# Kernel optimization log

Hardware: AMD Instinct MI355X
Metric: run time of the kernel (lower is better)

The kernel has to match this reference:

```python
import jax, jax.numpy as jnp
import numpy as np

B, T, D, F, E, K, L, S = 8, 1024, 512, 1024, 8, 2, 2, 64
SE, SH = 64, 128  # subject_embed_dim, style_hidden_dim


def setup_inputs() -> dict:
    key = jax.random.key(0)
    ks = jax.random.split(key, 16)
    r = lambda i, shape, s=0.05: (jax.random.normal(ks[i], shape, jnp.float32) * s)
    return dict(
        x=jax.random.normal(ks[0], (B, T, D), jnp.float32),
        subject_ids=jax.random.randint(ks[1], (B,), 0, S),
        # per-layer LayerNorm params (L, D)
        ln_g=jnp.ones((L, D), jnp.float32), ln_b=jnp.zeros((L, D), jnp.float32),
        # per-layer SubjectStyleAlignment params (weights stored (in, out))
        subj_emb=r(2, (L, S, SE), 0.02),
        h1_w=r(3, (L, SE, SH)), h1_b=jnp.zeros((L, SH), jnp.float32),
        h2_w=r(4, (L, SH, SH)), h2_b=jnp.zeros((L, SH), jnp.float32),
        s1_w=r(5, (L, SH, SH // 2)), s1_b=jnp.zeros((L, SH // 2), jnp.float32),
        s2_w=r(6, (L, SH // 2, 2 * D)), s2_b=jnp.zeros((L, 2 * D), jnp.float32),
        # shared TopKRouter: Linear(D, D//2) -> ReLU -> Linear(D//2, E)
        g1_w=r(7, (D, D // 2)), g1_b=jnp.zeros((D // 2,), jnp.float32),
        g2_w=r(8, (D // 2, E)), g2_b=jnp.zeros((E,), jnp.float32),
        # shared ExpertPool of GLU experts (no bias)
        wi0=r(9, (E, D, F)), wi1=r(10, (E, D, F)), wo=r(11, (E, F, D)),
    )


def _layernorm(x, g, b):
    m = x.mean(-1, keepdims=True)
    v = x.var(-1, keepdims=True)  # biased, matches torch LayerNorm
    return (x - m) / jnp.sqrt(v + 1e-5) * g + b


def reference(x, subject_ids, ln_g, ln_b, subj_emb, h1_w, h1_b, h2_w, h2_b,
              s1_w, s1_b, s2_w, s2_b, g1_w, g1_b, g2_w, g2_b, wi0, wi1, wo):
    Bs, Ts, Ds = x.shape
    for l in range(L):  # small fixed layer loop; expert pool + router are shared
        res = x
        h = _layernorm(x, ln_g[l], ln_b[l])
        # SubjectStyleAlignment: instance norm over time axis per (B, D) channel
        mu = h.mean(1, keepdims=True)
        var = h.var(1, keepdims=True)
        hn = (h - mu) / jnp.sqrt(var + 1e-8)
        e = subj_emb[l][subject_ids]                               # (B, SE)
        hh = jax.nn.relu(e @ h1_w[l] + h1_b[l]) @ h2_w[l] + h2_b[l]
        sp = jax.nn.relu(hh @ s1_w[l] + s1_b[l]) @ s2_w[l] + s2_b[l]  # (B, 2D)
        gamma = jax.nn.softplus(sp[:, :Ds]) + 1e-8
        beta = sp[:, Ds:]
        h = hn * gamma[:, None, :] + beta[:, None, :]
        # Router (shared across layers)
        hf = h.reshape(-1, Ds)                                     # (N, D)
        logits = jax.nn.relu(hf @ g1_w + g1_b) @ g2_w + g2_b       # (N, E)
        probs = jax.nn.softmax(logits, -1)
        gates, idx = jax.lax.top_k(probs, K)                       # (N, K)
        gates = gates / (gates.sum(-1, keepdims=True) + 1e-8)
        # combine weights: cw[n, e] = sum_k gates[n,k] * [idx[n,k]==e]
        cw = (jax.nn.one_hot(idx, E, dtype=hf.dtype) * gates[..., None]).sum(1)  # (N, E)
        # GLU experts, computed dense over E then gated-combined
        hid = jax.nn.relu(jnp.einsum('nd,edf->enf', hf, wi0)) \
              * jnp.einsum('nd,edf->enf', hf, wi1)                 # (E, N, F)
        eo = jnp.einsum('enf,efd->end', hid, wo)                   # (E, N, D)
        y = jnp.einsum('ne,end->nd', cw, eo)                       # (N, D)
        x = res + y.reshape(Bs, Ts, Ds)
    return x
```

## Files before the change

### kernel.cpp

```cpp
#include <hip/hip_runtime.h>

typedef unsigned short u16;
typedef unsigned int   u32;
typedef _Float16       f16;
typedef __attribute__((ext_vector_type(8))) _Float16 f16x8;
typedef __attribute__((ext_vector_type(4))) float    f32x4;
typedef __attribute__((ext_vector_type(4))) double   dbl4;

#define NSLOT_ 16384

__device__ __forceinline__ u16 f16bits(f16 h){ union{f16 f; u16 u;} x; x.f = h; return x.u; }

__device__ __forceinline__ void gl_lds16(const void* gptr, void* lptr){
  __builtin_amdgcn_global_load_lds((const __attribute__((address_space(1))) u32*)gptr,
                                   (__attribute__((address_space(3))) u32*)lptr, 16, 0, 0);
}

__device__ __forceinline__ int roff(int row, int lks){
  return ((row >> 1) << 6) + ((lks ^ ((row >> 1) & 3)) << 4) + ((row & 1) << 3);
}

__global__ __launch_bounds__(256) void ln_kernel(const float* __restrict__ x,
    const float* __restrict__ g, const float* __restrict__ bb, float* __restrict__ h){
  int n = blockIdx.x, t = threadIdx.x;
  const float* xr = x + ((size_t)n << 9);
  float2 v = *(const float2*)&xr[t*2];
  double vx = v.x, vy = v.y;
  double s = vx + vy;
  double q = vx*vx + vy*vy;
  #pragma unroll
  for (int o = 32; o > 0; o >>= 1){ s += __shfl_down(s, o, 64); q += __shfl_down(q, o, 64); }
  __shared__ double ls[4], lq_[4];
  __shared__ double sm, sv;
  int wid = t >> 6, lane = t & 63;
  if (lane == 0){ ls[wid] = s; lq_[wid] = q; }
  __syncthreads();
  if (t == 0){
    double S = ls[0]+ls[1]+ls[2]+ls[3], Q = lq_[0]+lq_[1]+lq_[2]+lq_[3];
    double mean = S * (1.0/512.0);
    double var  = Q * (1.0/512.0) - mean*mean;
    sm = mean; sv = 1.0/sqrt(var + 1e-5);
  }
  __syncthreads();
  double mean = sm, inv = sv;
  int d = t*2;
  float2 o;
  o.x = (float)((vx - mean)*inv*(double)g[d]   + (double)bb[d]);
  o.y = (float)((vy - mean)*inv*(double)g[d+1] + (double)bb[d+1]);
  *(float2*)&h[((size_t)n<<9) + d] = o;
}

__global__ __launch_bounds__(128) void gather_ln(const float* __restrict__ xin,
    const float* __restrict__ eo, const int* __restrict__ slot_of, const float* __restrict__ wv,
    const float* __restrict__ g, const float* __restrict__ bb,
    float* __restrict__ out, float* __restrict__ h){
  int n = blockIdx.x, t = threadIdx.x;
  int s0 = slot_of[2*n], s1 = slot_of[2*n+1];
  double w0 = wv[2*n], w1 = wv[2*n+1];
  float4 xi = *(const float4*)&xin[((size_t)n << 9) + t*4];
  float4 e0 = *(const float4*)&eo[((size_t)s0 << 9) + t*4];
  float4 e1 = *(const float4*)&eo[((size_t)s1 << 9) + t*4];
  double o0 = (double)xi.x + w0*(double)e0.x + w1*(double)e1.x;
  double o1 = (double)xi.y + w0*(double)e0.y + w1*(double)e1.y;
  double o2 = (double)xi.z + w0*(double)e0.z + w1*(double)e1.z;
  double o3 = (double)xi.w + w0*(double)e0.w + w1*(double)e1.w;
  float4 o; o.x = (float)o0; o.y = (float)o1; o.z = (float)o2; o.w = (float)o3;
  *(float4*)&out[((size_t)n << 9) + t*4] = o;
  double vx = o.x, vy = o.y, vz = o.z, vw = o.w;
  double s = vx+vy+vz+vw;
  double q = vx*vx+vy*vy+vz*vz+vw*vw;
  #pragma unroll
  for (int off = 32; off > 0; off >>= 1){ s += __shfl_down(s, off, 64); q += __shfl_down(q, off, 64); }
  __shared__ double ls[2], lq_[2];
  __shared__ double sm, sv;
  int wid = t >> 6, lane = t & 63;
  if (lane == 0){ ls[wid] = s; lq_[wid] = q; }
  __syncthreads();
  if (t == 0){
    double S = ls[0]+ls[1], Q = lq_[0]+lq_[1];
    double mean = S * (1.0/512.0);
    double var  = Q * (1.0/512.0) - mean*mean;
    sm = mean; sv = 1.0/sqrt(var + 1e-5);
  }
  __syncthreads();
  double mean = sm, inv = sv;
  int d = t*4;
  float4 ho;
  ho.x = (float)((vx - mean)*inv*(double)g[d]   + (double)bb[d]);
  ho.y = (float)((vy - mean)*inv*(double)g[d+1] + (double)bb[d+1]);
  ho.z = (float)((vz - mean)*inv*(double)g[d+2] + (double)bb[d+2]);
  ho.w = (float)((vw - mean)*inv*(double)g[d+3] + (double)bb[d+3]);
  *(float4*)&h[((size_t)n<<9) + d] = ho;
}

__global__ __launch_bounds__(256) void colstats(const float* __restrict__ h,
    double* __restrict__ cs, double* __restrict__ cq){
  int bid = blockIdx.x;
  int b = bid >> 3, ch = bid & 7;
  int t = threadIdx.x;
  int col = ch*64 + (t & 63);
  int tp = t >> 6;
  const float* base = h + ((size_t)b << 19);
  double s = 0.0, q = 0.0;
  for (int tt = tp; tt < 1024; tt += 4){
    double v = (double)base[((size_t)tt << 9) + col];
    s += v; q += v*v;
  }
  __shared__ double ls[4][64], lq[4][64];
  ls[tp][t & 63] = s; lq[tp][t & 63] = q;
  __syncthreads();
  if (tp == 0){
    double S = ls[0][t]+ls[1][t]+ls[2][t]+ls[3][t];
    double Q = lq[0][t]+lq[1][t]+lq[2][t]+lq[3][t];
    cs[(b<<9)+col] = S; cq[(b<<9)+col] = Q;
  }
}

__global__ __launch_bounds__(256) void subj_kernel(const int* __restrict__ sid,
    const float* __restrict__ semb,
    const float* __restrict__ h1w, const float* __restrict__ h1b,
    const float* __restrict__ h2w, const float* __restrict__ h2b,
    const float* __restrict__ s1w, const float* __restrict__ s1b,
    const float* __restrict__ s2w, const float* __restrict__ s2b,
    const double* __restrict__ cs, const double* __restrict__ cq,
    double* __restrict__ a64, double* __restrict__ c64, int l){
  __shared__ double ev[64], hid1[128], hh[128], sh[64], sp[1024];
  int t = threadIdx.x;
  int b = blockIdx.x;
  int s = sid[b];
  if (t < 64) ev[t] = (double)semb[l*4096 + s*64 + t];
  __syncthreads();
  if (t < 128){
    double acc = (double)h1b[l*128 + t];
    for (int i = 0; i < 64; ++i) acc += ev[i]*(double)h1w[l*8192 + i*128 + t];
    hid1[t] = acc > 0.0 ? acc : 0.0;
  }
  __syncthreads();
  if (t < 128){
    double acc = (double)h2b[l*128 + t];
    for (int i = 0; i < 128; ++i) acc += hid1[i]*(double)h2w[l*16384 + i*128 + t];
    hh[t] = acc;
  }
  __syncthreads();
  if (t < 64){
    double acc = (double)s1b[l*64 + t];
    for (int i = 0; i < 128; ++i) acc += hh[i]*(double)s1w[l*8192 + i*64 + t];
    sh[t] = acc > 0.0 ? acc : 0.0;
  }
  __syncthreads();
  for (int m = t; m < 1024; m += 256){
    double acc = (double)s2b[l*1024 + m];
    for (int j = 0; j < 64; ++j) acc += sh[j]*(double)s2w[l*65536 + j*1024 + m];
    sp[m] = acc;
  }
  __syncthreads();
  for (int d = t; d < 512; d += 256){
    double mu  = cs[(b<<9)+d] * (1.0/1024.0);
    double var = cq[(b<<9)+d] * (1.0/1024.0) - mu*mu;
    double inv = 1.0/sqrt(var + 1e-8);
    double spv = sp[d];
    double gamma = (spv > 30.0 ? spv : log1p(exp(spv))) + 1e-8;
    double beta  = sp[512 + d];
    double A = gamma * inv;
    a64[(b<<9)+d] = A;
    c64[(b<<9)+d] = beta - mu*A;
  }
}

__global__ __launch_bounds__(256) void hfcast(const float* __restrict__ h,
    const double* __restrict__ a64, const double* __restrict__ c64,
    u16* __restrict__ hfh, u16* __restrict__ hfl, int* __restrict__ counts){
  if (blockIdx.x == 0 && threadIdx.x < 16) counts[threadIdx.x] = 0;
  size_t i0 = ((size_t)blockIdx.x*256 + threadIdx.x) * 8;
  int n = (int)(i0 >> 9);
  int d0 = (int)(i0 & 511);
  int b = n >> 10;
  float4 x0 = *(const float4*)&h[i0];
  float4 x1 = *(const float4*)&h[i0 + 4];
  dbl4 a0 = *(const dbl4*)&a64[(b<<9) + d0];
  dbl4 a1 = *(const dbl4*)&a64[(b<<9) + d0 + 4];
  dbl4 c0 = *(const dbl4*)&c64[(b<<9) + d0];
  dbl4 c1 = *(const dbl4*)&c64[(b<<9) + d0 + 4];
  float f[8];
  f[0] = (float)((double)x0.x*a0[0] + c0[0]);
  f[1] = (float)((double)x0.y*a0[1] + c0[1]);
  f[2] = (float)((double)x0.z*a0[2] + c0[2]);
  f[3] = (float)((double)x0.w*a0[3] + c0[3]);
  f[4] = (float)((double)x1.x*a1[0] + c1[0]);
  f[5] = (float)((double)x1.y*a1[1] + c1[1]);
  f[6] = (float)((double)x1.z*a1[2] + c1[2]);
  f[7] = (float)((double)x1.w*a1[3] + c1[3]);
  ushort4 oh0, oh1, ol0, ol1;
  u16 vh[8], vl[8];
  #pragma unroll
  for (int j = 0; j < 8; ++j){
    f16 hi = (f16)f[j];
    float rem = (f[j] - (float)hi) * 2048.f;
    f16 lo = (f16)rem;
    vh[j] = f16bits(hi); vl[j] = f16bits(lo);
  }
  oh0.x=vh[0]; oh0.y=vh[1]; oh0.z=vh[2]; oh0.w=vh[3];
  oh1.x=vh[4]; oh1.y=vh[5]; oh1.z=vh[6]; oh1.w=vh[7];
  ol0.x=vl[0]; ol0.y=vl[1]; ol0.z=vl[2]; ol0.w=vl[3];
  ol1.x=vl[4]; ol1.y=vl[5]; ol1.z=vl[6]; ol1.w=vl[7];
  *(ushort4*)&hfh[i0]   = oh0;
  *(ushort4*)&hfh[i0+4] = oh1;
  *(ushort4*)&hfl[i0]   = ol0;
  *(ushort4*)&hfl[i0+4] = ol1;
}

__global__ __launch_bounds__(256) void gate2_kernel(const u16* __restrict__ hfh,
    const u16* __restrict__ hfl, const u16* __restrict__ g1Th, const u16* __restrict__ g1Tl,
    const float* __restrict__ g1b, const float* __restrict__ g2w, const float* __restrict__ g2b,
    int* __restrict__ idxo, float* __restrict__ wo_, int* __restrict__ counts){
  __shared__ double hid_s[16][258];
  __shared__ double lg[16*8];
  __shared__ int lcnt[8];
  int t = threadIdx.x, w = t >> 6, l = t & 63;
  int tok0 = blockIdx.x << 4;
  if (t < 8) lcnt[t] = 0;
  int lr = l & 15, lks = l >> 4;
  const u16* ahp = hfh + ((size_t)(tok0 + lr) << 9) + lks*8;
  const u16* alp = hfl + ((size_t)(tok0 + lr) << 9) + lks*8;
  const u16* bhp[4]; const u16* blp[4];
  #pragma unroll
  for (int nf = 0; nf < 4; ++nf){
    int col = w*64 + nf*16 + lr;
    bhp[nf] = g1Th + ((size_t)col << 9) + lks*8;
    blp[nf] = g1Tl + ((size_t)col << 9) + lks*8;
  }
  f32x4 hh[4], cr[4];
  #pragma unroll
  for (int nf = 0; nf < 4; ++nf)
    #pragma unroll
    for (int r = 0; r < 4; ++r){ hh[nf][r] = 0.f; cr[nf][r] = 0.f; }
  f16x8 ah = *(const f16x8*)ahp;
  f16x8 al = *(const f16x8*)alp;
  for (int kc = 0; kc < 512; kc += 32){
    int kn = (kc + 32) & 511;
    f16x8 ahn = *(const f16x8*)(ahp + kn);
    f16x8 aln = *(const f16x8*)(alp + kn);
    #pragma unroll
    for (int nf = 0; nf < 4; ++nf){
      f16x8 bh = *(const f16x8*)(bhp[nf] + kc);
      f16x8 bl = *(const f16x8*)(blp[nf] + kc);
      hh[nf] = __builtin_amdgcn_mfma_f32_16x16x32_f16(ah, bh, hh[nf], 0, 0, 0);
      cr[nf] = __builtin_amdgcn_mfma_f32_16x16x32_f16(ah, bl, cr[nf], 0, 0, 0);
      cr[nf] = __builtin_amdgcn_mfma_f32_16x16x32_f16(al, bh, cr[nf], 0, 0, 0);
    }
    ah = ahn; al = aln;
  }
  #pragma unroll
  for (int nf = 0; nf < 4; ++nf){
    int col = w*64 + nf*16 + lr;
    double gb = (double)g1b[col];
    #pragma unroll
    for (int r = 0; r < 4; ++r){
      int row = lks*4 + r;
      double v = (double)hh[nf][r] + (double)cr[nf][r]*(1.0/2048.0) + gb;
      hid_s[row][col] = v > 0.0 ? v : 0.0;
    }
  }
  __syncthreads();
  if (t < 128){
    int tok = t >> 3, e = t & 7;
    double la = (double)g2b[e];
    for (int k = 0; k < 256; ++k) la += hid_s[tok][k]*(double)g2w[(k<<3)+e];
    lg[(tok<<3)+e] = la;
  }
  __syncthreads();
  if (t < 16){
    double l0[8];
    #pragma unroll
    for (int e = 0; e < 8; ++e) l0[e] = lg[(t<<3)+e];
    double m = l0[0];
    #pragma unroll
    for (int e = 1; e < 8; ++e) m = fmax(m, l0[e]);
    double p[8]; double s = 0.0;
    #pragma unroll
    for (int e = 0; e < 8; ++e){ p[e] = exp(l0[e]-m); s += p[e]; }
    double b1 = -1e300, b2 = -1e300; int i1 = 0, i2 = 1;
    #pragma unroll
    for (int e = 0; e < 8; ++e){
      double v = l0[e];
      if (v > b1){ b2 = b1; i2 = i1; b1 = v; i1 = e; }
      else if (v > b2){ b2 = v; i2 = e; }
    }
    double pr1 = p[i1]/s, pr2 = p[i2]/s;
    double den = pr1 + pr2 + 1e-8;
    int n = tok0 + t;
    idxo[2*n] = i1; idxo[2*n+1] = i2;
    wo_[2*n] = (float)(pr1/den); wo_[2*n+1] = (float)(pr2/den);
    atomicAdd(&lcnt[i1], 1); atomicAdd(&lcnt[i2], 1);
  }
  __syncthreads();
  if (t < 8) atomicAdd(&counts[t], lcnt[t]);
}

__global__ __launch_bounds__(256) void scatter_kernel(const int* __restrict__ idx,
    const int* __restrict__ counts, int* __restrict__ cur,
    int* __restrict__ offs, int* __restrict__ tok_of, int* __restrict__ slot_of){
  __shared__ int lcnt[8], lbase[8], offs_s[8];
  int t = threadIdx.x;
  int n = blockIdx.x*256 + t;
  if (t < 8) lcnt[t] = 0;
  if (t == 0){
    int run = 0;
    for (int e = 0; e < 8; ++e){ offs_s[e] = run; run += counts[e]; }
  }
  __syncthreads();
  if (blockIdx.x == 0 && t < 8) offs[t] = offs_s[t];
  int e0 = idx[2*n], e1 = idx[2*n+1];
  int p0 = atomicAdd(&lcnt[e0], 1);
  int p1 = atomicAdd(&lcnt[e1], 1);
  __syncthreads();
  if (t < 8) lbase[t] = atomicAdd(&cur[t], lcnt[t]);
  __syncthreads();
  int s0 = offs_s[e0] + lbase[e0] + p0;
  int s1 = offs_s[e1] + lbase[e1] + p1;
  tok_of[s0] = n; tok_of[s1] = n;
  slot_of[2*n] = s0; slot_of[2*n+1] = s1;
}

__device__ __forceinline__ void cvt_tile(const float* __restrict__ src,
    u16* __restrict__ dh, u16* __restrict__ dl, int R, int C, int bx){
  int tilesC = C >> 5, tilesR = R >> 5;
  int e = bx / (tilesR*tilesC);
  int rem = bx % (tilesR*tilesC);
  int rt = rem / tilesC, ct = rem % tilesC;
  __shared__ float tile[32][33];
  int t = threadIdx.x;
  int j = t & 31, i0 = t >> 5;
  const float* s = src + (size_t)e*R*C + (size_t)(rt*32)*C + ct*32;
  for (int ii = i0; ii < 32; ii += 8) tile[ii][j] = s[(size_t)ii*C + j];
  __syncthreads();
  size_t ob = (size_t)e*R*C + (size_t)(ct*32)*R + rt*32;
  for (int ii = i0; ii < 32; ii += 8){
    float v = tile[j][ii];
    f16 hi = (f16)v;
    float rem2 = (v - (float)hi) * 2048.f;
    f16 lo = (f16)rem2;
    dh[ob + (size_t)ii*R + j] = f16bits(hi);
    dl[ob + (size_t)ii*R + j] = f16bits(lo);
  }
}

__global__ __launch_bounds__(256) void cvt_all(const float* __restrict__ wi0,
    const float* __restrict__ wi1, const float* __restrict__ wo, const float* __restrict__ g1w,
    u16* __restrict__ w0Th, u16* __restrict__ w0Tl, u16* __restrict__ w1Th, u16* __restrict__ w1Tl,
    u16* __restrict__ woTh, u16* __restrict__ woTl, u16* __restrict__ g1Th, u16* __restrict__ g1Tl){
  int bx = blockIdx.x;
  if (bx < 4096)       cvt_tile(wi0, w0Th, w0Tl, 512, 1024, bx);
  else if (bx < 8192)  cvt_tile(wi1, w1Th, w1Tl, 512, 1024, bx - 4096);
  else if (bx < 12288) cvt_tile(wo,  woTh, woTl, 1024, 512, bx - 8192);
  else                 cvt_tile(g1w, g1Th, g1Tl, 512, 256,  bx - 12288);
}

__global__ __launch_bounds__(256) void up1_kernel(const u16* __restrict__ hfh,
    const u16* __restrict__ hfl,
    const u16* __restrict__ w0h, const u16* __restrict__ w0l,
    const u16* __restrict__ w1h, const u16* __restrict__ w1l,
    const int* __restrict__ tok_of, const int* __restrict__ offs, const int* __restrict__ counts,
    u16* __restrict__ hidh, u16* __restrict__ hidl){
  int bx = blockIdx.x;
  int e  = bx >> 11;
  int mt = (bx >> 4) & 127;
  int nt = bx & 15;
  int base = offs[e], cnt = counts[e];
  int row0 = mt << 7;
  if (row0 >= cnt) return;
  __shared__ __align__(16) u16 Ah[2][4096], Alo[2][4096];
  __shared__ __align__(16) u16 B0h[2][2048], B0l[2][2048], B1h[2][2048], B1l[2][2048];
  int t = threadIdx.x, w = t >> 6, l = t & 63;
  int wm = w >> 1, wn = w & 1;
  int lr = l & 15, lks = l >> 4;
  int riw = ((l >> 3) << 1) | (l & 1);
  int kc16s = ((((l >> 1) & 3) ^ ((l >> 3) & 3)) << 3);
  int ar1 = w*16 + riw;
  int tokA1, tokA2;
  { int ss = base + row0 + ar1;      ss = ss < NSLOT_ ? ss : NSLOT_-1; tokA1 = tok_of[ss]; }
  { int ss = base + row0 + 64 + ar1; ss = ss < NSLOT_ ? ss : NSLOT_-1; tokA2 = tok_of[ss]; }
  const u16* sAh1 = hfh + ((size_t)tokA1 << 9) + kc16s;
  const u16* sAh2 = hfh + ((size_t)tokA2 << 9) + kc16s;
  const u16* sAl1 = hfl + ((size_t)tokA1 << 9) + kc16s;
  const u16* sAl2 = hfl + ((size_t)tokA2 << 9) + kc16s;
  size_t bcol = (size_t)(e*1024 + nt*64);
  size_t bci = (bcol + (size_t)ar1) << 9;
  const u16* sB0h = w0h + bci + kc16s;
  const u16* sB0l = w0l + bci + kc16s;
  const u16* sB1h = w1h + bci + kc16s;
  const u16* sB1l = w1l + bci + kc16s;
  int aoff[4], boff[2];
  #pragma unroll
  for (int mi = 0; mi < 4; ++mi) aoff[mi] = roff(wm*64 + mi*16 + lr, lks);
  #pragma unroll
  for (int ni = 0; ni < 2; ++ni) boff[ni] = roff(wn*32 + ni*16 + lr, lks);
  f32x4 hh0[4][2], cr0[4][2], hh1[4][2], cr1[4][2];
  #pragma unroll
  for (int i = 0; i < 4; ++i)
    #pragma unroll
    for (int j = 0; j < 2; ++j)
      #pragma unroll
      for (int r = 0; r < 4; ++r){ hh0[i][j][r]=0.f; cr0[i][j][r]=0.f; hh1[i][j][r]=0.f; cr1[i][j][r]=0.f; }
#define STG_U(buf, kc) do{ \
    gl_lds16(sAh1 + (kc), &Ah[buf][t*8]); \
    gl_lds16(sAh2 + (kc), &Ah[buf][2048 + t*8]); \
    gl_lds16(sAl1 + (kc), &Alo[buf][t*8]); \
    gl_lds16(sAl2 + (kc), &Alo[buf][2048 + t*8]); \
    gl_lds16(sB0h + (kc), &B0h[buf][t*8]); \
    gl_lds16(sB0l + (kc), &B0l[buf][t*8]); \
    gl_lds16(sB1h + (kc), &B1h[buf][t*8]); \
    gl_lds16(sB1l + (kc), &B1l[buf][t*8]); }while(0)
  STG_U(0, 0);
  for (int ks = 0; ks < 16; ++ks){
    int cur = ks & 1;
    __syncthreads();
    if (ks < 15) STG_U(cur^1, (ks+1)*32);
    f16x8 ah[4], al[4], b0hv[2], b0lv[2], b1hv[2], b1lv[2];
    #pragma unroll
    for (int mi = 0; mi < 4; ++mi){
      ah[mi] = *(const f16x8*)&Ah[cur][aoff[mi]];
      al[mi] = *(const f16x8*)&Alo[cur][aoff[mi]];
    }
    #pragma unroll
    for (int ni = 0; ni < 2; ++ni){
      b0hv[ni] = *(const f16x8*)&B0h[cur][boff[ni]];
      b0lv[ni] = *(const f16x8*)&B0l[cur][boff[ni]];
      b1hv[ni] = *(const f16x8*)&B1h[cur][boff[ni]];
      b1lv[ni] = *(const f16x8*)&B1l[cur][boff[ni]];
    }
    #pragma unroll
    for (int mi = 0; mi < 4; ++mi)
      #pragma unroll
      for (int ni = 0; ni < 2; ++ni){
        hh0[mi][ni] = __builtin_amdgcn_mfma_f32_16x16x32_f16(ah[mi], b0hv[ni], hh0[mi][ni], 0, 0, 0);
        hh1[mi][ni] = __builtin_amdgcn_mfma_f32_16x16x32_f16(ah[mi], b1hv[ni], hh1[mi][ni], 0, 0, 0);
        cr0[mi][ni] = __builtin_amdgcn_mfma_f32_16x16x32_f16(ah[mi], b0lv[ni], cr0[mi][ni], 0, 0, 0);
        cr0[mi][ni] = __builtin_amdgcn_mfma_f32_16x16x32_f16(al[mi], b0hv[ni], cr0[mi][ni], 0, 0, 0);
        cr1[mi][ni] = __builtin_amdgcn_mfma_f32_16x16x32_f16(ah[mi], b1lv[ni], cr1[mi][ni], 0, 0, 0);
        cr1[mi][ni] = __builtin_amdgcn_mfma_f32_16x16x32_f16(al[mi], b1hv[ni], cr1[mi][ni], 0, 0, 0);
      }
  }
#undef STG_U
  #pragma unroll
  for (int mi = 0; mi < 4; ++mi){
    int rb = row0 + wm*64 + mi*16 + lks*4;
    #pragma unroll
    for (int r = 0; r < 4; ++r){
      int rr = rb + r;
      if (rr < cnt){
        size_t orow = ((size_t)(base + rr) << 10) + nt*64;
        #pragma unroll
        for (int ni = 0; ni < 2; ++ni){
          int col = wn*32 + ni*16 + lr;
          float u0 = hh0[mi][ni][r] + cr0[mi][ni][r]*(1.f/2048.f);
          float u1 = hh1[mi][ni][r] + cr1[mi][ni][r]*(1.f/2048.f);
          u0 = u0 > 0.f ? u0 : 0.f;
          float v = u0*u1;
          f16 vh = (f16)v;
          float rem = (v - (float)vh)*2048.f;
          hidh[orow + col] = f16bits(vh);
          hidl[orow + col] = f16bits((f16)rem);
        }
      }
    }
  }
}

__global__ __launch_bounds__(256) void down1_kernel(const u16* __restrict__ hidh,
    const u16* __restrict__ hidl, const u16* __restrict__ wdh, const u16* __restrict__ wdl,
    const int* __restrict__ offs, const int* __restrict__ counts, float* __restrict__ eo){
  int bx = blockIdx.x;
  int e  = bx >> 10;
  int mt = (bx >> 3) & 127;
  int nt = bx & 7;
  int base = offs[e], cnt = counts[e];
  int row0 = mt << 7;
  if (row0 >= cnt) return;
  __shared__ __align__(16) u16 Ah[2][4096], Alo[2][4096];
  __shared__ __align__(16) u16 Bh[2][2048], Bl[2][2048];
  int t = threadIdx.x, w = t >> 6, l = t & 63;
  int wm = w >> 1, wn = w & 1;
  int lr = l & 15, lks = l >> 4;
  int riw = ((l >> 3) << 1) | (l & 1);
  int kc16s = ((((l >> 1) & 3) ^ ((l >> 3) & 3)) << 3);
  int ar1 = w*16 + riw;
  int sA1c = base + row0 + ar1;      sA1c = sA1c < NSLOT_ ? sA1c : NSLOT_-1;
  int sA2c = base + row0 + 64 + ar1; sA2c = sA2c < NSLOT_ ? sA2c : NSLOT_-1;
  const u16* sAh1 = hidh + ((size_t)sA1c << 10) + kc16s;
  const u16* sAh2 = hidh + ((size_t)sA2c << 10) + kc16s;
  const u16* sAl1 = hidl + ((size_t)sA1c << 10) + kc16s;
  const u16* sAl2 = hidl + ((size_t)sA2c << 10) + kc16s;
  size_t bcol = (size_t)(e*512 + nt*64);
  size_t bci = (bcol + (size_t)ar1) << 10;
  const u16* sBh = wdh + bci + kc16s;
  const u16* sBl = wdl + bci + kc16s;
  int aoff[4], boff[2];
  #pragma unroll
  for (int mi = 0; mi < 4; ++mi) aoff[mi] = roff(wm*64 + mi*16 + lr, lks);
  #pragma unroll
  for (int ni = 0; ni < 2; ++ni) boff[ni] = roff(wn*32 + ni*16 + lr, lks);
  f32x4 hh[4][2], cr[4][2];
  #pragma unroll
  for (int i = 0; i < 4; ++i)
    #pragma unroll
    for (int j = 0; j < 2; ++j)
      #pragma unroll
      for (int r = 0; r < 4; ++r){ hh[i][j][r]=0.f; cr[i][j][r]=0.f; }
#define STG_D(buf, kc) do{ \
    gl_lds16(sAh1 + (kc), &Ah[buf][t*8]); \
    gl_lds16(sAh2 + (kc), &Ah[buf][2048 + t*8]); \
    gl_lds16(sAl1 + (kc), &Alo[buf][t*8]); \
    gl_lds16(sAl2 + (kc), &Alo[buf][2048 + t*8]); \
    gl_lds16(sBh + (kc), &Bh[buf][t*8]); \
    gl_lds16(sBl + (kc), &Bl[buf][t*8]); }while(0)
  STG_D(0, 0);
  for (int ks = 0; ks < 32; ++ks){
    int cur = ks & 1;
    __syncthreads();
    if (ks < 31) STG_D(cur^1, (ks+1)*32);
    f16x8 ah[4], al[4], bh[2], bl[2];
    #pragma unroll
    for (int mi = 0; mi < 4; ++mi){
      ah[mi] = *(const f16x8*)&Ah[cur][aoff[mi]];
      al[mi] = *(const f16x8*)&Alo[cur][aoff[mi]];
    }
    #pragma unroll
    for (int ni = 0; ni < 2; ++ni){
      bh[ni] = *(const f16x8*)&Bh[cur][boff[ni]];
      bl[ni] = *(const f16x8*)&Bl[cur][boff[ni]];
    }
    #pragma unroll
    for (int mi = 0; mi < 4; ++mi)
      #pragma unroll
      for (int ni = 0; ni < 2; ++ni){
        hh[mi][ni] = __builtin_amdgcn_mfma_f32_16x16x32_f16(ah[mi], bh[ni], hh[mi][ni], 0, 0, 0);
        cr[mi][ni] = __builtin_amdgcn_mfma_f32_16x16x32_f16(ah[mi], bl[ni], cr[mi][ni], 0, 0, 0);
        cr[mi][ni] = __builtin_amdgcn_mfma_f32_16x16x32_f16(al[mi], bh[ni], cr[mi][ni], 0, 0, 0);
      }
  }
#undef STG_D
  #pragma unroll
  for (int mi = 0; mi < 4; ++mi){
    int rb = row0 + wm*64 + mi*16 + lks*4;
    #pragma unroll
    for (int r = 0; r < 4; ++r){
      int rr = rb + r;
      if (rr < cnt){
        float* orow = eo + (((size_t)(base + rr)) << 9) + nt*64;
        #pragma unroll
        for (int ni = 0; ni < 2; ++ni)
          orow[wn*32 + ni*16 + lr] = hh[mi][ni][r] + cr[mi][ni][r]*(1.f/2048.f);
      }
    }
  }
}

__global__ __launch_bounds__(256) void uph_kernel(const u16* __restrict__ hfh,
    const u16* __restrict__ w0h, const u16* __restrict__ w1h,
    const int* __restrict__ tok_of, const int* __restrict__ offs, const int* __restrict__ counts,
    u16* __restrict__ hidh){
  int bx = blockIdx.x;
  int e  = bx >> 10;
  int mt = (bx >> 3) & 127;
  int nt = bx & 7;
  int base = offs[e], cnt = counts[e];
  int row0 = mt << 7;
  if (row0 >= cnt) return;
  __shared__ __align__(16) u16 Ah[2][4096];
  __shared__ __align__(16) u16 B0[2][4096], B1[2][4096];
  int t = threadIdx.x, w = t >> 6, l = t & 63;
  int wm = w >> 1, wn = w & 1;
  int lr = l & 15, lks = l >> 4;
  int riw = ((l >> 3) << 1) | (l & 1);
  int kc16s = ((((l >> 1) & 3) ^ ((l >> 3) & 3)) << 3);
  int ar1 = w*16 + riw;
  int tokA1, tokA2;
  { int ss = base + row0 + ar1;      ss = ss < NSLOT_ ? ss : NSLOT_-1; tokA1 = tok_of[ss]; }
  { int ss = base + row0 + 64 + ar1; ss = ss < NSLOT_ ? ss : NSLOT_-1; tokA2 = tok_of[ss]; }
  const u16* sAh1 = hfh + ((size_t)tokA1 << 9) + kc16s;
  const u16* sAh2 = hfh + ((size_t)tokA2 << 9) + kc16s;
  size_t bcol = (size_t)(e*1024 + nt*128);
  const u16* sB0a = w0h + ((bcol + (size_t)ar1) << 9) + kc16s;
  const u16* sB0b = w0h + ((bcol + 64 + (size_t)ar1) << 9) + kc16s;
  const u16* sB1a = w1h + ((bcol + (size_t)ar1) << 9) + kc16s;
  const u16* sB1b = w1h + ((bcol + 64 + (size_t)ar1) << 9) + kc16s;
  int aoff[4], boff[4];
  #pragma unroll
  for (int mi = 0; mi < 4; ++mi) aoff[mi] = roff(wm*64 + mi*16 + lr, lks);
  #pragma unroll
  for (int ni = 0; ni < 4; ++ni) boff[ni] = roff(wn*64 + ni*16 + lr, lks);
  f32x4 hh0[4][4], hh1[4][4];
  #pragma unroll
  for (int i = 0; i < 4; ++i)
    #pragma unroll
    for (int j = 0; j < 4; ++j)
      #pragma unroll
      for (int r = 0; r < 4; ++r){ hh0[i][j][r]=0.f; hh1[i][j][r]=0.f; }
#define STG_UH(buf, kc) do{ \
    gl_lds16(sAh1 + (kc), &Ah[buf][t*8]); \
    gl_lds16(sAh2 + (kc), &Ah[buf][2048 + t*8]); \
    gl_lds16(sB0a + (kc), &B0[buf][t*8]); \
    gl_lds16(sB0b + (kc), &B0[buf][2048 + t*8]); \
    gl_lds16(sB1a + (kc), &B1[buf][t*8]); \
    gl_lds16(sB1b + (kc), &B1[buf][2048 + t*8]); }while(0)
  STG_UH(0, 0);
  for (int ks = 0; ks < 16; ++ks){
    int cur = ks & 1;
    __syncthreads();
    if (ks < 15) STG_UH(cur^1, (ks+1)*32);
    f16x8 ah[4], b0v[4], b1v[4];
    #pragma unroll
    for (int mi = 0; mi < 4; ++mi) ah[mi] = *(const f16x8*)&Ah[cur][aoff[mi]];
    #pragma unroll
    for (int ni = 0; ni < 4; ++ni){
      b0v[ni] = *(const f16x8*)&B0[cur][boff[ni]];
      b1v[ni] = *(const f16x8*)&B1[cur][boff[ni]];
    }
    #pragma unroll
    for (int mi = 0; mi < 4; ++mi)
      #pragma unroll
      for (int ni = 0; ni < 4; ++ni){
        hh0[mi][ni] = __builtin_amdgcn_mfma_f32_16x16x32_f16(ah[mi], b0v[ni], hh0[mi][ni], 0, 0, 0);
        hh1[mi][ni] = __builtin_amdgcn_mfma_f32_16x16x32_f16(ah[mi], b1v[ni], hh1[mi][ni], 0, 0, 0);
      }
  }
#undef STG_UH
  #pragma unroll
  for (int mi = 0; mi < 4; ++mi){
    int rb = row0 + wm*64 + mi*16 + lks*4;
    #pragma unroll
    for (int r = 0; r < 4; ++r){
      int rr = rb + r;
      if (rr < cnt){
        size_t orow = ((size_t)(base + rr) << 10) + nt*128;
        #pragma unroll
        for (int ni = 0; ni < 4; ++ni){
          int col = wn*64 + ni*16 + lr;
          float u0 = hh0[mi][ni][r];
          u0 = u0 > 0.f ? u0 : 0.f;
          hidh[orow + col] = f16bits((f16)(u0*hh1[mi][ni][r]));
        }
      }
    }
  }
}

__global__ __launch_bounds__(256) void dnh_kernel(const u16* __restrict__ hidh,
    const u16* __restrict__ wdh,
    const int* __restrict__ offs, const int* __restrict__ counts, float* __restrict__ eo){
  int bx = blockIdx.x;
  int e  = bx >> 9;
  int mt = (bx >> 2) & 127;
  int nt = bx & 3;
  int base = offs[e], cnt = counts[e];
  int row0 = mt << 7;
  if (row0 >= cnt) return;
  __shared__ __align__(16) u16 Ah[2][4096];
  __shared__ __align__(16) u16 Bh[2][4096];
  int t = threadIdx.x, w = t >> 6, l = t & 63;
  int wm = w >> 1, wn = w & 1;
  int lr = l & 15, lks = l >> 4;
  int riw = ((l >> 3) << 1) | (l & 1);
  int kc16s = ((((l >> 1) & 3) ^ ((l >> 3) & 3)) << 3);
  int ar1 = w*16 + riw;
  int sA1c = base + row0 + ar1;      sA1c = sA1c < NSLOT_ ? sA1c : NSLOT_-1;
  int sA2c = base + row0 + 64 + ar1; sA2c = sA2c < NSLOT_ ? sA2c : NSLOT_-1;
  const u16* sAh1 = hidh + ((size_t)sA1c << 10) + kc16s;
  const u16* sAh2 = hidh + ((size_t)sA2c << 10) + kc16s;
  size_t bcol = (size_t)(e*512 + nt*128);
  const u16* sB1 = wdh + ((bcol + (size_t)ar1) << 10) + kc16s;
  const u16* sB2 = wdh + ((bcol + 64 + (size_t)ar1) << 10) + kc16s;
  int aoff[4], boff[4];
  #pragma unroll
  for (int mi = 0; mi < 4; ++mi) aoff[mi] = roff(wm*64 + mi*16 + lr, lks);
  #pragma unroll
  for (int ni = 0; ni < 4; ++ni) boff[ni] = roff(wn*64 + ni*16 + lr, lks);
  f32x4 hh[4][4];
  #pragma unroll
  for (int i = 0; i < 4; ++i)
    #pragma unroll
    for (int j = 0; j < 4; ++j)
      #pragma unroll
      for (int r = 0; r < 4; ++r) hh[i][j][r] = 0.f;
#define STG_DH(buf, kc) do{ \
    gl_lds16(sAh1 + (kc), &Ah[buf][t*8]); \
    gl_lds16(sAh2 + (kc), &Ah[buf][2048 + t*8]); \
    gl_lds16(sB1 + (kc), &Bh[buf][t*8]); \
    gl_lds16(sB2 + (kc), &Bh[buf][2048 + t*8]); }while(0)
  STG_DH(0, 0);
  for (int ks = 0; ks < 32; ++ks){
    int cur = ks & 1;
    __syncthreads();
    if (ks < 31) STG_DH(cur^1, (ks+1)*32);
    f16x8 ah[4], bh[4];
    #pragma unroll
    for (int mi = 0; mi < 4; ++mi) ah[mi] = *(const f16x8*)&Ah[cur][aoff[mi]];
    #pragma unroll
    for (int ni = 0; ni < 4; ++ni) bh[ni] = *(const f16x8*)&Bh[cur][boff[ni]];
    #pragma unroll
    for (int mi = 0; mi < 4; ++mi)
      #pragma unroll
      for (int ni = 0; ni < 4; ++ni)
        hh[mi][ni] = __builtin_amdgcn_mfma_f32_16x16x32_f16(ah[mi], bh[ni], hh[mi][ni], 0, 0, 0);
  }
#undef STG_DH
  #pragma unroll
  for (int mi = 0; mi < 4; ++mi){
    int rb = row0 + wm*64 + mi*16 + lks*4;
    #pragma unroll
    for (int r = 0; r < 4; ++r){
      int rr = rb + r;
      if (rr < cnt){
        float* orow = eo + (((size_t)(base + rr)) << 9) + nt*128;
        #pragma unroll
        for (int ni = 0; ni < 4; ++ni)
          orow[wn*64 + ni*16 + lr] = hh[mi][ni][r];
      }
    }
  }
}

__global__ __launch_bounds__(128) void gather_kernel(const float* __restrict__ xin,
    const float* __restrict__ eo, const int* __restrict__ slot_of, const float* __restrict__ wv,
    float* __restrict__ out){
  int n = blockIdx.x, t = threadIdx.x;
  int s0 = slot_of[2*n], s1 = slot_of[2*n+1];
  double w0 = wv[2*n], w1 = wv[2*n+1];
  float4 xi = *(const float4*)&xin[((size_t)n << 9) + t*4];
  float4 e0 = *(const float4*)&eo[((size_t)s0 << 9) + t*4];
  float4 e1 = *(const float4*)&eo[((size_t)s1 << 9) + t*4];
  float4 o;
  o.x = (float)((double)xi.x + w0*(double)e0.x + w1*(double)e1.x);
  o.y = (float)((double)xi.y + w0*(double)e0.y + w1*(double)e1.y);
  o.z = (float)((double)xi.z + w0*(double)e0.z + w1*(double)e1.z);
  o.w = (float)((double)xi.w + w0*(double)e0.w + w1*(double)e1.w);
  *(float4*)&out[((size_t)n << 9) + t*4] = o;
}

extern "C" void kernel_launch(void* const* d_in, const int* in_sizes, int n_in,
                              void* d_out, int out_size, void* d_ws, size_t ws_size,
                              hipStream_t stream) {
  (void)in_sizes; (void)n_in; (void)out_size; (void)ws_size;
  const float* x0   = (const float*)d_in[0];
  const int*   sid  = (const int*)  d_in[1];
  const float* ln_g = (const float*)d_in[2];
  const float* ln_b = (const float*)d_in[3];
  const float* semb = (const float*)d_in[4];
  const float* h1w  = (const float*)d_in[5];
  const float* h1b  = (const float*)d_in[6];
  const float* h2w  = (const float*)d_in[7];
  const float* h2b  = (const float*)d_in[8];
  const float* s1w  = (const float*)d_in[9];
  const float* s1b  = (const float*)d_in[10];
  const float* s2w  = (const float*)d_in[11];
  const float* s2b  = (const float*)d_in[12];
  const float* g1w  = (const float*)d_in[13];
  const float* g1b  = (const float*)d_in[14];
  const float* g2w  = (const float*)d_in[15];
  const float* g2b  = (const float*)d_in[16];
  const float* wi0  = (const float*)d_in[17];
  const float* wi1  = (const float*)d_in[18];
  const float* wo   = (const float*)d_in[19];

  char* W = (char*)d_ws;
  float*  h      = (float*)(W + 0);
  u16*    hfh    = (u16*)  (W + 16777216ULL);
  u16*    hfl    = (u16*)  (W + 25165824ULL);
  float*  eo32   = (float*)(W + 167772160ULL);
  u16*    hid16h = (u16*)  (W + 33554432ULL);
  u16*    hid16l = (u16*)  (W + 67108864ULL);
  u16*    w0Th   = (u16*)  (W + 100663296ULL);
  u16*    w0Tl   = (u16*)  (W + 109051904ULL);
  u16*    w1Th   = (u16*)  (W + 117440512ULL);
  u16*    w1Tl   = (u16*)  (W + 125829120ULL);
  u16*    woTh   = (u16*)  (W + 134217728ULL);
  u16*    woTl   = (u16*)  (W + 142606336ULL);
  u16*    g1Th   = (u16*)  (W + 150994944ULL);
  u16*    g1Tl   = (u16*)  (W + 151257088ULL);
  double* cs     = (double*)(W + 151519232ULL);
  double* cq     = (double*)(W + 151552000ULL);
  double* a64    = (double*)(W + 151584768ULL);
  double* c64    = (double*)(W + 151617536ULL);
  int*    idxa   = (int*)   (W + 151650304ULL);
  float*  warr   = (float*) (W + 151715840ULL);
  int*    tok_of = (int*)   (W + 151781376ULL);
  int*    slot_of= (int*)   (W + 151846912ULL);
  int*    counts = (int*)   (W + 151912448ULL);
  int*    cur    = counts + 8;
  int*    offs   = counts + 16;

  cvt_all<<<12416, 256, 0, stream>>>(wi0, wi1, wo, g1w,
                                     w0Th, w0Tl, w1Th, w1Tl, woTh, woTl, g1Th, g1Tl);

  ln_kernel<<<8192, 256, 0, stream>>>(x0, ln_g, ln_b, h);
  colstats<<<64, 256, 0, stream>>>(h, cs, cq);
  subj_kernel<<<8, 256, 0, stream>>>(sid, semb, h1w, h1b, h2w, h2b, s1w, s1b, s2w, s2b,
                                     cs, cq, a64, c64, 0);
  hfcast<<<2048, 256, 0, stream>>>(h, a64, c64, hfh, hfl, counts);
  gate2_kernel<<<512, 256, 0, stream>>>(hfh, hfl, g1Th, g1Tl, g1b, g2w, g2b, idxa, warr, counts);
  scatter_kernel<<<32, 256, 0, stream>>>(idxa, counts, cur, offs, tok_of, slot_of);
  up1_kernel<<<16384, 256, 0, stream>>>(hfh, hfl, w0Th, w0Tl, w1Th, w1Tl,
                                        tok_of, offs, counts, hid16h, hid16l);
  down1_kernel<<<8192, 256, 0, stream>>>(hid16h, hid16l, woTh, woTl, offs, counts, eo32);
  gather_ln<<<8192, 128, 0, stream>>>(x0, eo32, slot_of, warr, ln_g + 512, ln_b + 512,
                                      (float*)d_out, h);
  colstats<<<64, 256, 0, stream>>>(h, cs, cq);
  subj_kernel<<<8, 256, 0, stream>>>(sid, semb, h1w, h1b, h2w, h2b, s1w, s1b, s2w, s2b,
                                     cs, cq, a64, c64, 1);
  hfcast<<<2048, 256, 0, stream>>>(h, a64, c64, hfh, hfl, counts);
  gate2_kernel<<<512, 256, 0, stream>>>(hfh, hfl, g1Th, g1Tl, g1b, g2w, g2b, idxa, warr, counts);
  scatter_kernel<<<32, 256, 0, stream>>>(idxa, counts, cur, offs, tok_of, slot_of);
  uph_kernel<<<8192, 256, 0, stream>>>(hfh, w0Th, w1Th, tok_of, offs, counts, hid16h);
  dnh_kernel<<<4096, 256, 0, stream>>>(hid16h, woTh, offs, counts, eo32);
  gather_kernel<<<8192, 128, 0, stream>>>((const float*)d_out, eo32, slot_of, warr, (float*)d_out);
}
```

Measured before the change: 884.5 us.

## Persistent expert GEMM blocks with strided M-tile loops and split column stats

The expert up/down GEMM kernels switch from a launch sized for the worst case (128 M-tiles per expert, most exiting early) to a fixed grid of 16 blocks per expert and N-tile, each looping over M-tiles with stride 16. This removes thousands of empty blocks that only launched and returned. Colstats is split over 8 time chunks into partial sums that subj_kernel reduces, giving more parallelism than the old 64-block launch. The gate logits loop splits K in half across all 256 threads. The trade-off is a load imbalance risk when one expert gets many more tokens than the others.

After: 1.070 ms. 21.0% more time.

```diff
diff --git a/kernel.cpp b/kernel.cpp
--- a/kernel.cpp
+++ b/kernel.cpp
@@ -94,15 +94,17 @@
 }
 
 __global__ __launch_bounds__(256) void colstats(const float* __restrict__ h,
-    double* __restrict__ cs, double* __restrict__ cq){
+    double* __restrict__ pS, double* __restrict__ pQ){
   int bid = blockIdx.x;
-  int b = bid >> 3, ch = bid & 7;
+  int b  = bid >> 6;
+  int ch = (bid >> 3) & 7;
+  int tc = bid & 7;
   int t = threadIdx.x;
   int col = ch*64 + (t & 63);
   int tp = t >> 6;
-  const float* base = h + ((size_t)b << 19);
+  const float* base = h + ((size_t)b << 19) + ((size_t)(tc*128) << 9);
   double s = 0.0, q = 0.0;
-  for (int tt = tp; tt < 1024; tt += 4){
+  for (int tt = tp; tt < 128; tt += 4){
     double v = (double)base[((size_t)tt << 9) + col];
     s += v; q += v*v;
   }
@@ -112,7 +114,8 @@
   if (tp == 0){
     double S = ls[0][t]+ls[1][t]+ls[2][t]+ls[3][t];
     double Q = lq[0][t]+lq[1][t]+lq[2][t]+lq[3][t];
-    cs[(b<<9)+col] = S; cq[(b<<9)+col] = Q;
+    pS[((tc<<3)+b)*512 + col] = S;
+    pQ[((tc<<3)+b)*512 + col] = Q;
   }
 }
 
@@ -122,11 +125,21 @@
     const float* __restrict__ h2w, const float* __restrict__ h2b,
     const float* __restrict__ s1w, const float* __restrict__ s1b,
     const float* __restrict__ s2w, const float* __restrict__ s2b,
-    const double* __restrict__ cs, const double* __restrict__ cq,
+    const double* __restrict__ pS, const double* __restrict__ pQ,
     double* __restrict__ a64, double* __restrict__ c64, int l){
   __shared__ double ev[64], hid1[128], hh[128], sh[64], sp[1024];
+  __shared__ double cs_s[512], cq_s[512];
   int t = threadIdx.x;
   int b = blockIdx.x;
+  for (int d = t; d < 512; d += 256){
+    double S = 0.0, Q = 0.0;
+    #pragma unroll
+    for (int tc = 0; tc < 8; ++tc){
+      S += pS[((tc<<3)+b)*512 + d];
+      Q += pQ[((tc<<3)+b)*512 + d];
+    }
+    cs_s[d] = S; cq_s[d] = Q;
+  }
   int s = sid[b];
   if (t < 64) ev[t] = (double)semb[l*4096 + s*64 + t];
   __syncthreads();
@@ -155,8 +168,8 @@
   }
   __syncthreads();
   for (int d = t; d < 512; d += 256){
-    double mu  = cs[(b<<9)+d] * (1.0/1024.0);
-    double var = cq[(b<<9)+d] * (1.0/1024.0) - mu*mu;
+    double mu  = cs_s[d] * (1.0/1024.0);
+    double var = cq_s[d] * (1.0/1024.0) - mu*mu;
     double inv = 1.0/sqrt(var + 1e-8);
     double spv = sp[d];
     double gamma = (spv > 30.0 ? spv : log1p(exp(spv))) + 1e-8;
@@ -215,6 +228,7 @@
     int* __restrict__ idxo, float* __restrict__ wo_, int* __restrict__ counts){
   __shared__ double hid_s[16][258];
   __shared__ double lg[16*8];
+  __shared__ double lg2[256];
   __shared__ int lcnt[8];
   int t = threadIdx.x, w = t >> 6, l = t & 63;
   int tok0 = blockIdx.x << 4;
@@ -262,12 +276,16 @@
     }
   }
   __syncthreads();
-  if (t < 128){
-    int tok = t >> 3, e = t & 7;
-    double la = (double)g2b[e];
-    for (int k = 0; k < 256; ++k) la += hid_s[tok][k]*(double)g2w[(k<<3)+e];
-    lg[(tok<<3)+e] = la;
-  }
+  {
+    int pair = t >> 1, kh = t & 1;
+    int tok = pair >> 3, e = pair & 7;
+    double la = kh ? 0.0 : (double)g2b[e];
+    int k0 = kh << 7;
+    for (int k = k0; k < k0 + 128; ++k) la += hid_s[tok][k]*(double)g2w[(k<<3)+e];
+    lg2[t] = la;
+  }
+  __syncthreads();
+  if (t < 128) lg[t] = lg2[2*t] + lg2[2*t+1];
   __syncthreads();
   if (t < 16){
     double l0[8];
@@ -363,12 +381,10 @@
     const int* __restrict__ tok_of, const int* __restrict__ offs, const int* __restrict__ counts,
     u16* __restrict__ hidh, u16* __restrict__ hidl){
   int bx = blockIdx.x;
-  int e  = bx >> 11;
-  int mt = (bx >> 4) & 127;
-  int nt = bx & 15;
+  int e  = bx >> 8;
+  int nt = (bx >> 4) & 15;
+  int st = bx & 15;
   int base = offs[e], cnt = counts[e];
-  int row0 = mt << 7;
-  if (row0 >= cnt) return;
   __shared__ __align__(16) u16 Ah[2][4096], Alo[2][4096];
   __shared__ __align__(16) u16 B0h[2][2048], B0l[2][2048], B1h[2][2048], B1l[2][2048];
   int t = threadIdx.x, w = t >> 6, l = t & 63;
@@ -377,13 +393,6 @@
   int riw = ((l >> 3) << 1) | (l & 1);
   int kc16s = ((((l >> 1) & 3) ^ ((l >> 3) & 3)) << 3);
   int ar1 = w*16 + riw;
-  int tokA1, tokA2;
-  { int ss = base + row0 + ar1;      ss = ss < NSLOT_ ? ss : NSLOT_-1; tokA1 = tok_of[ss]; }
-  { int ss = base + row0 + 64 + ar1; ss = ss < NSLOT_ ? ss : NSLOT_-1; tokA2 = tok_of[ss]; }
-  const u16* sAh1 = hfh + ((size_t)tokA1 << 9) + kc16s;
-  const u16* sAh2 = hfh + ((size_t)tokA2 << 9) + kc16s;
-  const u16* sAl1 = hfl + ((size_t)tokA1 << 9) + kc16s;
-  const u16* sAl2 = hfl + ((size_t)tokA2 << 9) + kc16s;
   size_t bcol = (size_t)(e*1024 + nt*64);
   size_t bci = (bcol + (size_t)ar1) << 9;
   const u16* sB0h = w0h + bci + kc16s;
@@ -395,13 +404,23 @@
   for (int mi = 0; mi < 4; ++mi) aoff[mi] = roff(wm*64 + mi*16 + lr, lks);
   #pragma unroll
   for (int ni = 0; ni < 2; ++ni) boff[ni] = roff(wn*32 + ni*16 + lr, lks);
-  f32x4 hh0[4][2], cr0[4][2], hh1[4][2], cr1[4][2];
-  #pragma unroll
-  for (int i = 0; i < 4; ++i)
-    #pragma unroll
-    for (int j = 0; j < 2; ++j)
-      #pragma unroll
-      for (int r = 0; r < 4; ++r){ hh0[i][j][r]=0.f; cr0[i][j][r]=0.f; hh1[i][j][r]=0.f; cr1[i][j][r]=0.f; }
+
+  for (int mt = st; (mt << 7) < cnt; mt += 16){
+    int row0 = mt << 7;
+    int tokA1, tokA2;
+    { int ss = base + row0 + ar1;      ss = ss < NSLOT_ ? ss : NSLOT_-1; tokA1 = tok_of[ss]; }
+    { int ss = base + row0 + 64 + ar1; ss = ss < NSLOT_ ? ss : NSLOT_-1; tokA2 = tok_of[ss]; }
+    const u16* sAh1 = hfh + ((size_t)tokA1 << 9) + kc16s;
+    const u16* sAh2 = hfh + ((size_t)tokA2 << 9) + kc16s;
+    const u16* sAl1 = hfl + ((size_t)tokA1 << 9) + kc16s;
+    const u16* sAl2 = hfl + ((size_t)tokA2 << 9) + kc16s;
+    f32x4 hh0[4][2], cr0[4][2], hh1[4][2], cr1[4][2];
+    #pragma unroll
+    for (int i = 0; i < 4; ++i)
+      #pragma unroll
+      for (int j = 0; j < 2; ++j)
+        #pragma unroll
+        for (int r = 0; r < 4; ++r){ hh0[i][j][r]=0.f; cr0[i][j][r]=0.f; hh1[i][j][r]=0.f; cr1[i][j][r]=0.f; }
 #define STG_U(buf, kc) do{ \
     gl_lds16(sAh1 + (kc), &Ah[buf][t*8]); \
     gl_lds16(sAh2 + (kc), &Ah[buf][2048 + t*8]); \
@@ -411,56 +430,57 @@
     gl_lds16(sB0l + (kc), &B0l[buf][t*8]); \
     gl_lds16(sB1h + (kc), &B1h[buf][t*8]); \
     gl_lds16(sB1l + (kc), &B1l[buf][t*8]); }while(0)
-  STG_U(0, 0);
-  for (int ks = 0; ks < 16; ++ks){
-    int cur = ks & 1;
-    __syncthreads();
-    if (ks < 15) STG_U(cur^1, (ks+1)*32);
-    f16x8 ah[4], al[4], b0hv[2], b0lv[2], b1hv[2], b1lv[2];
-    #pragma unroll
-    for (int mi = 0; mi < 4; ++mi){
-      ah[mi] = *(const f16x8*)&Ah[cur][aoff[mi]];
-      al[mi] = *(const f16x8*)&Alo[cur][aoff[mi]];
-    }
-    #pragma unroll
-    for (int ni = 0; ni < 2; ++ni){
-      b0hv[ni] = *(const f16x8*)&B0h[cur][boff[ni]];
-      b0lv[ni] = *(const f16x8*)&B0l[cur][boff[ni]];
-      b1hv[ni] = *(const f16x8*)&B1h[cur][boff[ni]];
-      b1lv[ni] = *(const f16x8*)&B1l[cur][boff[ni]];
-    }
-    #pragma unroll
-    for (int mi = 0; mi < 4; ++mi)
+    STG_U(0, 0);
+    for (int ks = 0; ks < 16; ++ks){
+      int cur = ks & 1;
+      __syncthreads();
+      if (ks < 15) STG_U(cur^1, (ks+1)*32);
+      f16x8 ah[4], al[4], b0hv[2], b0lv[2], b1hv[2], b1lv[2];
+      #pragma unroll
+      for (int mi = 0; mi < 4; ++mi){
+        ah[mi] = *(const f16x8*)&Ah[cur][aoff[mi]];
+        al[mi] = *(const f16x8*)&Alo[cur][aoff[mi]];
+      }
       #pragma unroll
       for (int ni = 0; ni < 2; ++ni){
-        hh0[mi][ni] = __builtin_amdgcn_mfma_f32_16x16x32_f16(ah[mi], b0hv[ni], hh0[mi][ni], 0, 0, 0);
-        hh1[mi][ni] = __builtin_amdgcn_mfma_f32_16x16x32_f16(ah[mi], b1hv[ni], hh1[mi][ni], 0, 0, 0);
-        cr0[mi][ni] = __builtin_amdgcn_mfma_f32_16x16x32_f16(ah[mi], b0lv[ni], cr0[mi][ni], 0, 0, 0);
-        cr0[mi][ni] = __builtin_amdgcn_mfma_f32_16x16x32_f16(al[mi], b0hv[ni], cr0[mi][ni], 0, 0, 0);
-        cr1[mi][ni] = __builtin_amdgcn_mfma_f32_16x16x32_f16(ah[mi], b1lv[ni], cr1[mi][ni], 0, 0, 0);
-        cr1[mi][ni] = __builtin_amdgcn_mfma_f32_16x16x32_f16(al[mi], b1hv[ni], cr1[mi][ni], 0, 0, 0);
+        b0hv[ni] = *(const f16x8*)&B0h[cur][boff[ni]];
+        b0lv[ni] = *(const f16x8*)&B0l[cur][boff[ni]];
+        b1hv[ni] = *(const f16x8*)&B1h[cur][boff[ni]];
+        b1lv[ni] = *(const f16x8*)&B1l[cur][boff[ni]];
       }
-  }
-#undef STG_U
-  #pragma unroll
-  for (int mi = 0; mi < 4; ++mi){
-    int rb = row0 + wm*64 + mi*16 + lks*4;
-    #pragma unroll
-    for (int r = 0; r < 4; ++r){
-      int rr = rb + r;
-      if (rr < cnt){
-        size_t orow = ((size_t)(base + rr) << 10) + nt*64;
+      #pragma unroll
+      for (int mi = 0; mi < 4; ++mi)
         #pragma unroll
         for (int ni = 0; ni < 2; ++ni){
-          int col = wn*32 + ni*16 + lr;
-          float u0 = hh0[mi][ni][r] + cr0[mi][ni][r]*(1.f/2048.f);
-          float u1 = hh1[mi][ni][r] + cr1[mi][ni][r]*(1.f/2048.f);
-          u0 = u0 > 0.f ? u0 : 0.f;
-          float v = u0*u1;
-          f16 vh = (f16)v;
-          float rem = (v - (float)vh)*2048.f;
-          hidh[orow + col] = f16bits(vh);
-          hidl[orow + col] = f16bits((f16)rem);
+          hh0[mi][ni] = __builtin_amdgcn_mfma_f32_16x16x32_f16(ah[mi], b0hv[ni], hh0[mi][ni], 0, 0, 0);
+          hh1[mi][ni] = __builtin_amdgcn_mfma_f32_16x16x32_f16(ah[mi], b1hv[ni], hh1[mi][ni], 0, 0, 0);
+          cr0[mi][ni] = __builtin_amdgcn_mfma_f32_16x16x32_f16(ah[mi], b0lv[ni], cr0[mi][ni], 0, 0, 0);
+          cr0[mi][ni] = __builtin_amdgcn_mfma_f32_16x16x32_f16(al[mi], b0hv[ni], cr0[mi][ni], 0, 0, 0);
+          cr1[mi][ni] = __builtin_amdgcn_mfma_f32_16x16x32_f16(ah[mi], b1lv[ni], cr1[mi][ni], 0, 0, 0);
+          cr1[mi][ni] = __builtin_amdgcn_mfma_f32_16x16x32_f16(al[mi], b1hv[ni], cr1[mi][ni], 0, 0, 0);
+        }
+    }
+#undef STG_U
+    #pragma unroll
+    for (int mi = 0; mi < 4; ++mi){
+      int rb = row0 + wm*64 + mi*16 + lks*4;
+      #pragma unroll
+      for (int r = 0; r < 4; ++r){
+        int rr = rb + r;
+        if (rr < cnt){
+          size_t orow = ((size_t)(base + rr) << 10) + nt*64;
+          #pragma unroll
+          for (int ni = 0; ni < 2; ++ni){
+            int col = wn*32 + ni*16 + lr;
+            float u0 = hh0[mi][ni][r] + cr0[mi][ni][r]*(1.f/2048.f);
+            float u1 = hh1[mi][ni][r] + cr1[mi][ni][r]*(1.f/2048.f);
+            u0 = u0 > 0.f ? u0 : 0.f;
+            float v = u0*u1;
+            f16 vh = (f16)v;
+            float rem = (v - (float)vh)*2048.f;
+            hidh[orow + col] = f16bits(vh);
+            hidl[orow + col] = f16bits((f16)rem);
+          }
         }
       }
     }
@@ -471,12 +491,10 @@
     const u16* __restrict__ hidl, const u16* __restrict__ wdh, const u16* __restrict__ wdl,
     const int* __restrict__ offs, const int* __restrict__ counts, float* __restrict__ eo){
   int bx = blockIdx.x;
-  int e  = bx >> 10;
-  int mt = (bx >> 3) & 127;
-  int nt = bx & 7;
+  int e  = bx >> 7;
+  int nt = (bx >> 4) & 7;
+  int st = bx & 15;
   int base = offs[e], cnt = counts[e];
-  int row0 = mt << 7;
-  if (row0 >= cnt) return;
   __shared__ __align__(16) u16 Ah[2][4096], Alo[2][4096];
   __shared__ __align__(16) u16 Bh[2][2048], Bl[2][2048];
   int t = threadIdx.x, w = t >> 6, l = t & 63;
@@ -485,12 +503,6 @@
   int riw = ((l >> 3) << 1) | (l & 1);
   int kc16s = ((((l >> 1) & 3) ^ ((l >> 3) & 3)) << 3);
   int ar1 = w*16 + riw;
-  int sA1c = base + row0 + ar1;      sA1c = sA1c < NSLOT_ ? sA1c : NSLOT_-1;
-  int sA2c = base + row0 + 64 + ar1; sA2c = sA2c < NSLOT_ ? sA2c : NSLOT_-1;
-  const u16* sAh1 = hidh + ((size_t)sA1c << 10) + kc16s;
-  const u16* sAh2 = hidh + ((size_t)sA2c << 10) + kc16s;
-  const u16* sAl1 = hidl + ((size_t)sA1c << 10) + kc16s;
-  const u16* sAl2 = hidl + ((size_t)sA2c << 10) + kc16s;
   size_t bcol = (size_t)(e*512 + nt*64);
   size_t bci = (bcol + (size_t)ar1) << 10;
   const u16* sBh = wdh + bci + kc16s;
@@ -500,13 +512,22 @@
   for (int mi = 0; mi < 4; ++mi) aoff[mi] = roff(wm*64 + mi*16 + lr, lks);
   #pragma unroll
   for (int ni = 0; ni < 2; ++ni) boff[ni] = roff(wn*32 + ni*16 + lr, lks);
-  f32x4 hh[4][2], cr[4][2];
-  #pragma unroll
-  for (int i = 0; i < 4; ++i)
-    #pragma unroll
-    for (int j = 0; j < 2; ++j)
-      #pragma unroll
-      for (int r = 0; r < 4; ++r){ hh[i][j][r]=0.f; cr[i][j][r]=0.f; }
+
+  for (int mt = st; (mt << 7) < cnt; mt += 16){
+    int row0 = mt << 7;
+    int sA1c = base + row0 + ar1;      sA1c = sA1c < NSLOT_ ? sA1c : NSLOT_-1;
+    int sA2c = base + row0 + 64 + ar1; sA2c = sA2c < NSLOT_ ? sA2c : NSLOT_-1;
+    const u16* sAh1 = hidh + ((size_t)sA1c << 10) + kc16s;
+    const u16* sAh2 = hidh + ((size_t)sA2c << 10) + kc16s;
+    const u16* sAl1 = hidl + ((size_t)sA1c << 10) + kc16s;
+    const u16* sAl2 = hidl + ((size_t)sA2c << 10) + kc16s;
+    f32x4 hh[4][2], cr[4][2];
+    #pragma unroll
+    for (int i = 0; i < 4; ++i)
+      #pragma unroll
+      for (int j = 0; j < 2; ++j)
+        #pragma unroll
+        for (int r = 0; r < 4; ++r){ hh[i][j][r]=0.f; cr[i][j][r]=0.f; }
 #define STG_D(buf, kc) do{ \
     gl_lds16(sAh1 + (kc), &Ah[buf][t*8]); \
     gl_lds16(sAh2 + (kc), &Ah[buf][2048 + t*8]); \
@@ -514,43 +535,44 @@
     gl_lds16(sAl2 + (kc), &Alo[buf][2048 + t*8]); \
     gl_lds16(sBh + (kc), &Bh[buf][t*8]); \
     gl_lds16(sBl + (kc), &Bl[buf][t*8]); }while(0)
-  STG_D(0, 0);
-  for (int ks = 0; ks < 32; ++ks){
-    int cur = ks & 1;
-    __syncthreads();
-    if (ks < 31) STG_D(cur^1, (ks+1)*32);
-    f16x8 ah[4], al[4], bh[2], bl[2];
+    STG_D(0, 0);
+    for (int ks = 0; ks < 32; ++ks){
+      int cur = ks & 1;
+      __syncthreads();
+      if (ks < 31) STG_D(cur^1, (ks+1)*32);
+      f16x8 ah[4], al[4], bh[2], bl[2];
+      #pragma unroll
+      for (int mi = 0; mi < 4; ++mi){
+        ah[mi] = *(const f16x8*)&Ah[cur][aoff[mi]];
+        al[mi] = *(const f16x8*)&Alo[cur][aoff[mi]];
+      }
+      #pragma unroll
+      for (int ni = 0; ni < 2; ++ni){
+        bh[ni] = *(const f16x8*)&Bh[cur][boff[ni]];
+        bl[ni] = *(const f16x8*)&Bl[cur][boff[ni]];
+      }
+      #pragma unroll
+      for (int mi = 0; mi < 4; ++mi)
+        #pragma unroll
+        for (int ni = 0; ni < 2; ++ni){
+          hh[mi][ni] = __builtin_amdgcn_mfma_f32_16x16x32_f16(ah[mi], bh[ni], hh[mi][ni], 0, 0, 0);
+          cr[mi][ni] = __builtin_amdgcn_mfma_f32_16x16x32_f16(ah[mi], bl[ni], cr[mi][ni], 0, 0, 0);
+          cr[mi][ni] = __builtin_amdgcn_mfma_f32_16x16x32_f16(al[mi], bh[ni], cr[mi][ni], 0, 0, 0);
+        }
+    }
+#undef STG_D
     #pragma unroll
     for (int mi = 0; mi < 4; ++mi){
-      ah[mi] = *(const f16x8*)&Ah[cur][aoff[mi]];
-      al[mi] = *(const f16x8*)&Alo[cur][aoff[mi]];
-    }
-    #pragma unroll
-    for (int ni = 0; ni < 2; ++ni){
-      bh[ni] = *(const f16x8*)&Bh[cur][boff[ni]];
-      bl[ni] = *(const f16x8*)&Bl[cur][boff[ni]];
-    }
-    #pragma unroll
-    for (int mi = 0; mi < 4; ++mi)
-      #pragma unroll
-      for (int ni = 0; ni < 2; ++ni){
-        hh[mi][ni] = __builtin_amdgcn_mfma_f32_16x16x32_f16(ah[mi], bh[ni], hh[mi][ni], 0, 0, 0);
-        cr[mi][ni] = __builtin_amdgcn_mfma_f32_16x16x32_f16(ah[mi], bl[ni], cr[mi][ni], 0, 0, 0);
-        cr[mi][ni] = __builtin_amdgcn_mfma_f32_16x16x32_f16(al[mi], bh[ni], cr[mi][ni], 0, 0, 0);
-      }
-  }
-#undef STG_D
-  #pragma unroll
-  for (int mi = 0; mi < 4; ++mi){
-    int rb = row0 + wm*64 + mi*16 + lks*4;
-    #pragma unroll
-    for (int r = 0; r < 4; ++r){
-      int rr = rb + r;
-      if (rr < cnt){
-        float* orow = eo + (((size_t)(base + rr)) << 9) + nt*64;
-        #pragma unroll
-        for (int ni = 0; ni < 2; ++ni)
-          orow[wn*32 + ni*16 + lr] = hh[mi][ni][r] + cr[mi][ni][r]*(1.f/2048.f);
+      int rb = row0 + wm*64 + mi*16 + lks*4;
+      #pragma unroll
+      for (int r = 0; r < 4; ++r){
+        int rr = rb + r;
+        if (rr < cnt){
+          float* orow = eo + (((size_t)(base + rr)) << 9) + nt*64;
+          #pragma unroll
+          for (int ni = 0; ni < 2; ++ni)
+            orow[wn*32 + ni*16 + lr] = hh[mi][ni][r] + cr[mi][ni][r]*(1.f/2048.f);
+        }
       }
     }
   }
@@ -561,12 +583,10 @@
     const int* __restrict__ tok_of, const int* __restrict__ offs, const int* __restrict__ counts,
     u16* __restrict__ hidh){
   int bx = blockIdx.x;
-  int e  = bx >> 10;
-  int mt = (bx >> 3) & 127;
-  int nt = bx & 7;
+  int e  = bx >> 7;
+  int nt = (bx >> 4) & 7;
+  int st = bx & 15;
   int base = offs[e], cnt = counts[e];
-  int row0 = mt << 7;
-  if (row0 >= cnt) return;
   __shared__ __align__(16) u16 Ah[2][4096];
   __shared__ __align__(16) u16 B0[2][4096], B1[2][4096];
   int t = threadIdx.x, w = t >> 6, l = t & 63;
@@ -575,11 +595,6 @@
   int riw = ((l >> 3) << 1) | (l & 1);
   int kc16s = ((((l >> 1) & 3) ^ ((l >> 3) & 3)) << 3);
   int ar1 = w*16 + riw;
-  int tokA1, tokA2;
-  { int ss = base + row0 + ar1;      ss = ss < NSLOT_ ? ss : NSLOT_-1; tokA1 = tok_of[ss]; }
-  { int ss = base + row0 + 64 + ar1; ss = ss < NSLOT_ ? ss : NSLOT_-1; tokA2 = tok_of[ss]; }
-  const u16* sAh1 = hfh + ((size_t)tokA1 << 9) + kc16s;
-  const u16* sAh2 = hfh + ((size_t)tokA2 << 9) + kc16s;
   size_t bcol = (size_t)(e*1024 + nt*128);
   const u16* sB0a = w0h + ((bcol + (size_t)ar1) << 9) + kc16s;
   const u16* sB0b = w0h + ((bcol + 64 + (size_t)ar1) << 9) + kc16s;
@@ -590,13 +605,21 @@
   for (int mi = 0; mi < 4; ++mi) aoff[mi] = roff(wm*64 + mi*16 + lr, lks);
   #pragma unroll
   for (int ni = 0; ni < 4; ++ni) boff[ni] = roff(wn*64 + ni*16 + lr, lks);
-  f32x4 hh0[4][4], hh1[4][4];
-  #pragma unroll
-  for (int i = 0; i < 4; ++i)
-    #pragma unroll
-    for (int j = 0; j < 4; ++j)
-      #pragma unroll
-      for (int r = 0; r < 4; ++r){ hh0[i][j][r]=0.f; hh1[i][j][r]=0.f; }
+
+  for (int mt = st; (mt << 7) < cnt; mt += 16){
+    int row0 = mt << 7;
+    int tokA1, tokA2;
+    { int ss = base + row0 + ar1;      ss = ss < NSLOT_ ? ss : NSLOT_-1; tokA1 = tok_of[ss]; }
+    { int ss = base + row0 + 64 + ar1; ss = ss < NSLOT_ ? ss : NSLOT_-1; tokA2 = tok_of[ss]; }
+    const u16* sAh1 = hfh + ((size_t)tokA1 << 9) + kc16s;
+    const u16* sAh2 = hfh + ((size_t)tokA2 << 9) + kc16s;
+    f32x4 hh0[4][4], hh1[4][4];
+    #pragma unroll
+    for (int i = 0; i < 4; ++i)
+      #pragma unroll
+      for (int j = 0; j < 4; ++j)
+        #pragma unroll
+        for (int r = 0; r < 4; ++r){ hh0[i][j][r]=0.f; hh1[i][j][r]=0.f; }
 #define STG_UH(buf, kc) do{ \
     gl_lds16(sAh1 + (kc), &Ah[buf][t*8]); \
     gl_lds16(sAh2 + (kc), &Ah[buf][2048 + t*8]); \
@@ -604,42 +627,43 @@
     gl_lds16(sB0b + (kc), &B0[buf][2048 + t*8]); \
     gl_lds16(sB1a + (kc), &B1[buf][t*8]); \
     gl_lds16(sB1b + (kc), &B1[buf][2048 + t*8]); }while(0)
-  STG_UH(0, 0);
-  for (int ks = 0; ks < 16; ++ks){
-    int cur = ks & 1;
-    __syncthreads();
-    if (ks < 15) STG_UH(cur^1, (ks+1)*32);
-    f16x8 ah[4], b0v[4], b1v[4];
-    #pragma unroll
-    for (int mi = 0; mi < 4; ++mi) ah[mi] = *(const f16x8*)&Ah[cur][aoff[mi]];
-    #pragma unroll
-    for (int ni = 0; ni < 4; ++ni){
-      b0v[ni] = *(const f16x8*)&B0[cur][boff[ni]];
-      b1v[ni] = *(const f16x8*)&B1[cur][boff[ni]];
-    }
-    #pragma unroll
-    for (int mi = 0; mi < 4; ++mi)
+    STG_UH(0, 0);
+    for (int ks = 0; ks < 16; ++ks){
+      int cur = ks & 1;
+      __syncthreads();
+      if (ks < 15) STG_UH(cur^1, (ks+1)*32);
+      f16x8 ah[4], b0v[4], b1v[4];
+      #pragma unroll
+      for (int mi = 0; mi < 4; ++mi) ah[mi] = *(const f16x8*)&Ah[cur][aoff[mi]];
       #pragma unroll
       for (int ni = 0; ni < 4; ++ni){
-        hh0[mi][ni] = __builtin_amdgcn_mfma_f32_16x16x32_f16(ah[mi], b0v[ni], hh0[mi][ni], 0, 0, 0);
-        hh1[mi][ni] = __builtin_amdgcn_mfma_f32_16x16x32_f16(ah[mi], b1v[ni], hh1[mi][ni], 0, 0, 0);
+        b0v[ni] = *(const f16x8*)&B0[cur][boff[ni]];
+        b1v[ni] = *(const f16x8*)&B1[cur][boff[ni]];
       }
-  }
-#undef STG_UH
-  #pragma unroll
-  for (int mi = 0; mi < 4; ++mi){
-    int rb = row0 + wm*64 + mi*16 + lks*4;
-    #pragma unroll
-    for (int r = 0; r < 4; ++r){
-      int rr = rb + r;
-      if (rr < cnt){
-        size_t orow = ((size_t)(base + rr) << 10) + nt*128;
+      #pragma unroll
+      for (int mi = 0; mi < 4; ++mi)
         #pragma unroll
         for (int ni = 0; ni < 4; ++ni){
-          int col = wn*64 + ni*16 + lr;
-          float u0 = hh0[mi][ni][r];
-          u0 = u0 > 0.f ? u0 : 0.f;
-          hidh[orow + col] = f16bits((f16)(u0*hh1[mi][ni][r]));
+          hh0[mi][ni] = __builtin_amdgcn_mfma_f32_16x16x32_f16(ah[mi], b0v[ni], hh0[mi][ni], 0, 0, 0);
+          hh1[mi][ni] = __builtin_amdgcn_mfma_f32_16x16x32_f16(ah[mi], b1v[ni], hh1[mi][ni], 0, 0, 0);
+        }
+    }
+#undef STG_UH
+    #pragma unroll
+    for (int mi = 0; mi < 4; ++mi){
+      int rb = row0 + wm*64 + mi*16 + lks*4;
+      #pragma unroll
+      for (int r = 0; r < 4; ++r){
+        int rr = rb + r;
+        if (rr < cnt){
+          size_t orow = ((size_t)(base + rr) << 10) + nt*128;
+          #pragma unroll
+          for (int ni = 0; ni < 4; ++ni){
+            int col = wn*64 + ni*16 + lr;
+            float u0 = hh0[mi][ni][r];
+            u0 = u0 > 0.f ? u0 : 0.f;
+            hidh[orow + col] = f16bits((f16)(u0*hh1[mi][ni][r]));
+          }
         }
       }
     }
@@ -650,12 +674,10 @@
     const u16* __restrict__ wdh,
     const int* __restrict__ offs, const int* __restrict__ counts, float* __restrict__ eo){
   int bx = blockIdx.x;
-  int e  = bx >> 9;
-  int mt = (bx >> 2) & 127;
-  int nt = bx & 3;
+  int e  = bx >> 6;
+  int nt = (bx >> 4) & 3;
+  int st = bx & 15;
   int base = offs[e], cnt = counts[e];
-  int row0 = mt << 7;
-  if (row0 >= cnt) return;
   __shared__ __align__(16) u16 Ah[2][4096];
   __shared__ __align__(16) u16 Bh[2][4096];
   int t = threadIdx.x, w = t >> 6, l = t & 63;
@@ -664,10 +686,6 @@
   int riw = ((l >> 3) << 1) | (l & 1);
   int kc16s = ((((l >> 1) & 3) ^ ((l >> 3) & 3)) << 3);
   int ar1 = w*16 + riw;
-  int sA1c = base + row0 + ar1;      sA1c = sA1c < NSLOT_ ? sA1c : NSLOT_-1;
-  int sA2c = base + row0 + 64 + ar1; sA2c = sA2c < NSLOT_ ? sA2c : NSLOT_-1;
-  const u16* sAh1 = hidh + ((size_t)sA1c << 10) + kc16s;
-  const u16* sAh2 = hidh + ((size_t)sA2c << 10) + kc16s;
   size_t bcol = (size_t)(e*512 + nt*128);
   const u16* sB1 = wdh + ((bcol + (size_t)ar1) << 10) + kc16s;
   const u16* sB2 = wdh + ((bcol + 64 + (size_t)ar1) << 10) + kc16s;
@@ -676,46 +694,54 @@
   for (int mi = 0; mi < 4; ++mi) aoff[mi] = roff(wm*64 + mi*16 + lr, lks);
   #pragma unroll
   for (int ni = 0; ni < 4; ++ni) boff[ni] = roff(wn*64 + ni*16 + lr, lks);
-  f32x4 hh[4][4];
-  #pragma unroll
-  for (int i = 0; i < 4; ++i)
-    #pragma unroll
-    for (int j = 0; j < 4; ++j)
-      #pragma unroll
-      for (int r = 0; r < 4; ++r) hh[i][j][r] = 0.f;
+
+  for (int mt = st; (mt << 7) < cnt; mt += 16){
+    int row0 = mt << 7;
+    int sA1c = base + row0 + ar1;      sA1c = sA1c < NSLOT_ ? sA1c : NSLOT_-1;
+    int sA2c = base + row0 + 64 + ar1; sA2c = sA2c < NSLOT_ ? sA2c : NSLOT_-1;
+    const u16* sAh1 = hidh + ((size_t)sA1c << 10) + kc16s;
+    const u16* sAh2 = hidh + ((size_t)sA2c << 10) + kc16s;
+    f32x4 hh[4][4];
+    #pragma unroll
+    for (int i = 0; i < 4; ++i)
+      #pragma unroll
+      for (int j = 0; j < 4; ++j)
+        #pragma unroll
+        for (int r = 0; r < 4; ++r) hh[i][j][r] = 0.f;
 #define STG_DH(buf, kc) do{ \
     gl_lds16(sAh1 + (kc), &Ah[buf][t*8]); \
     gl_lds16(sAh2 + (kc), &Ah[buf][2048 + t*8]); \
     gl_lds16(sB1 + (kc), &Bh[buf][t*8]); \
     gl_lds16(sB2 + (kc), &Bh[buf][2048 + t*8]); }while(0)
-  STG_DH(0, 0);
-  for (int ks = 0; ks < 32; ++ks){
-    int cur = ks & 1;
-    __syncthreads();
-    if (ks < 31) STG_DH(cur^1, (ks+1)*32);
-    f16x8 ah[4], bh[4];
-    #pragma unroll
-    for (int mi = 0; mi < 4; ++mi) ah[mi] = *(const f16x8*)&Ah[cur][aoff[mi]];
-    #pragma unroll
-    for (int ni = 0; ni < 4; ++ni) bh[ni] = *(const f16x8*)&Bh[cur][boff[ni]];
-    #pragma unroll
-    for (int mi = 0; mi < 4; ++mi)
-      #pragma unroll
-      for (int ni = 0; ni < 4; ++ni)
-        hh[mi][ni] = __builtin_amdgcn_mfma_f32_16x16x32_f16(ah[mi], bh[ni], hh[mi][ni], 0, 0, 0);
-  }
-#undef STG_DH
-  #pragma unroll
-  for (int mi = 0; mi < 4; ++mi){
-    int rb = row0 + wm*64 + mi*16 + lks*4;
-    #pragma unroll
-    for (int r = 0; r < 4; ++r){
-      int rr = rb + r;
-      if (rr < cnt){
-        float* orow = eo + (((size_t)(base + rr)) << 9) + nt*128;
+    STG_DH(0, 0);
+    for (int ks = 0; ks < 32; ++ks){
+      int cur = ks & 1;
+      __syncthreads();
+      if (ks < 31) STG_DH(cur^1, (ks+1)*32);
+      f16x8 ah[4], bh[4];
+      #pragma unroll
+      for (int mi = 0; mi < 4; ++mi) ah[mi] = *(const f16x8*)&Ah[cur][aoff[mi]];
+      #pragma unroll
+      for (int ni = 0; ni < 4; ++ni) bh[ni] = *(const f16x8*)&Bh[cur][boff[ni]];
+      #pragma unroll
+      for (int mi = 0; mi < 4; ++mi)
         #pragma unroll
         for (int ni = 0; ni < 4; ++ni)
-          orow[wn*64 + ni*16 + lr] = hh[mi][ni][r];
+          hh[mi][ni] = __builtin_amdgcn_mfma_f32_16x16x32_f16(ah[mi], bh[ni], hh[mi][ni], 0, 0, 0);
+    }
+#undef STG_DH
+    #pragma unroll
+    for (int mi = 0; mi < 4; ++mi){
+      int rb = row0 + wm*64 + mi*16 + lks*4;
+      #pragma unroll
+      for (int r = 0; r < 4; ++r){
+        int rr = rb + r;
+        if (rr < cnt){
+          float* orow = eo + (((size_t)(base + rr)) << 9) + nt*128;
+          #pragma unroll
+          for (int ni = 0; ni < 4; ++ni)
+            orow[wn*64 + ni*16 + lr] = hh[mi][ni][r];
+        }
       }
     }
   }
@@ -778,8 +804,6 @@
   u16*    woTl   = (u16*)  (W + 142606336ULL);
   u16*    g1Th   = (u16*)  (W + 150994944ULL);
   u16*    g1Tl   = (u16*)  (W + 151257088ULL);
-  double* cs     = (double*)(W + 151519232ULL);
-  double* cq     = (double*)(W + 151552000ULL);
   double* a64    = (double*)(W + 151584768ULL);
   double* c64    = (double*)(W + 151617536ULL);
   int*    idxa   = (int*)   (W + 151650304ULL);
@@ -789,29 +813,31 @@
   int*    counts = (int*)   (W + 151912448ULL);
   int*    cur    = counts + 8;
   int*    offs   = counts + 16;
+  double* partS  = (double*)(W + 152043520ULL);
+  double* partQ  = (double*)(W + 152305664ULL);
 
   cvt_all<<<12416, 256, 0, stream>>>(wi0, wi1, wo, g1w,
                                      w0Th, w0Tl, w1Th, w1Tl, woTh, woTl, g1Th, g1Tl);
 
   ln_kernel<<<8192, 256, 0, stream>>>(x0, ln_g, ln_b, h);
-  colstats<<<64, 256, 0, stream>>>(h, cs, cq);
+  colstats<<<512, 256, 0, stream>>>(h, partS, partQ);
   subj_kernel<<<8, 256, 0, stream>>>(sid, semb, h1w, h1b, h2w, h2b, s1w, s1b, s2w, s2b,
-                                     cs, cq, a64, c64, 0);
+                                     partS, partQ, a64, c64, 0);
   hfcast<<<2048, 256, 0, stream>>>(h, a64, c64, hfh, hfl, counts);
   gate2_kernel<<<512, 256, 0, stream>>>(hfh, hfl, g1Th, g1Tl, g1b, g2w, g2b, idxa, warr, counts);
   scatter_kernel<<<32, 256, 0, stream>>>(idxa, counts, cur, offs, tok_of, slot_of);
-  up1_kernel<<<16384, 256, 0, stream>>>(hfh, hfl, w0Th, w0Tl, w1Th, w1Tl,
-                                        tok_of, offs, counts, hid16h, hid16l);
-  down1_kernel<<<8192, 256, 0, stream>>>(hid16h, hid16l, woTh, woTl, offs, counts, eo32);
+  up1_kernel<<<2048, 256, 0, stream>>>(hfh, hfl, w0Th, w0Tl, w1Th, w1Tl,
+                                       tok_of, offs, counts, hid16h, hid16l);
+  down1_kernel<<<1024, 256, 0, stream>>>(hid16h, hid16l, woTh, woTl, offs, counts, eo32);
   gather_ln<<<8192, 128, 0, stream>>>(x0, eo32, slot_of, warr, ln_g + 512, ln_b + 512,
                                       (float*)d_out, h);
-  colstats<<<64, 256, 0, stream>>>(h, cs, cq);
+  colstats<<<512, 256, 0, stream>>>(h, partS, partQ);
   subj_kernel<<<8, 256, 0, stream>>>(sid, semb, h1w, h1b, h2w, h2b, s1w, s1b, s2w, s2b,
-                                     cs, cq, a64, c64, 1);
+                                     partS, partQ, a64, c64, 1);
   hfcast<<<2048, 256, 0, stream>>>(h, a64, c64, hfh, hfl, counts);
   gate2_kernel<<<512, 256, 0, stream>>>(hfh, hfl, g1Th, g1Tl, g1b, g2w, g2b, idxa, warr, counts);
   scatter_kernel<<<32, 256, 0, stream>>>(idxa, counts, cur, offs, tok_of, slot_of);
-  uph_kernel<<<8192, 256, 0, stream>>>(hfh, w0Th, w1Th, tok_of, offs, counts, hid16h);
-  dnh_kernel<<<4096, 256, 0, stream>>>(hid16h, woTh, offs, counts, eo32);
+  uph_kernel<<<1024, 256, 0, stream>>>(hfh, w0Th, w1Th, tok_of, offs, counts, hid16h);
+  dnh_kernel<<<512, 256, 0, stream>>>(hid16h, woTh, offs, counts, eo32);
   gather_kernel<<<8192, 128, 0, stream>>>((const float*)d_out, eo32, slot_of, warr, (float*)d_out);
 }
```
